# Kernel optimization log

Measured on AMD Instinct MI355X. Metric: run time of the kernel, lower is better.

## Reference

```python
import jax, jax.numpy as jnp
import numpy as np

B, FEAT, Q, L, H_ENC, H_DEC = 256, 64, 16, 2, 128, 256


def _apply_1q(state, U, q):
    # state: [B, 2,2,...,2] (Q qubit axes); U: [B,2,2] complex64
    s = jnp.moveaxis(state, 1 + q, 1)
    shp = s.shape
    s2 = s.reshape(shp[0], 2, -1)
    s2 = jnp.einsum('bij,bjr->bir', U, s2)
    return jnp.moveaxis(s2.reshape(shp), 1, 1 + q)


def _apply_cnot(state, c, t):
    # flip target axis on the control=1 slice
    c0 = jnp.take(state, 0, axis=1 + c)
    c1 = jnp.take(state, 1, axis=1 + c)
    t_ax = 1 + t if t < c else t  # target axis index after removing control axis
    c1 = jnp.flip(c1, axis=t_ax)
    return jnp.stack([c0, c1], axis=1 + c)


def _u3(theta, phi, lam):
    # combined Rz(lam) @ Ry(phi) @ Rx(theta); inputs [B] -> [B,2,2] complex64
    j = jnp.complex64(1j)
    ct, st = jnp.cos(theta / 2), jnp.sin(theta / 2)
    cp, sp = jnp.cos(phi / 2), jnp.sin(phi / 2)
    Rx = jnp.stack([jnp.stack([ct + 0j, -j * st], -1),
                    jnp.stack([-j * st, ct + 0j], -1)], -2)
    Ry = jnp.stack([jnp.stack([cp + 0j, -sp + 0j], -1),
                    jnp.stack([sp + 0j, cp + 0j], -1)], -2)
    em, ep = jnp.exp(-j * lam / 2), jnp.exp(j * lam / 2)
    zero = jnp.zeros_like(em)
    Rz = jnp.stack([jnp.stack([em, zero], -1),
                    jnp.stack([zero, ep], -1)], -2)
    return jnp.einsum('bij,bjk,bkl->bil', Rz, Ry, Rx).astype(jnp.complex64)


def setup_inputs() -> dict:
    key = jax.random.key(0)
    ks = jax.random.split(key, 6)

    def xavier(k, shape):
        lim = float(np.sqrt(6.0 / (shape[0] + shape[1])))
        return jax.random.uniform(k, shape, jnp.float32, -lim, lim)

    return {
        'x': jax.random.normal(ks[0], (B, FEAT), jnp.float32),
        'W1': xavier(ks[1], (FEAT, H_ENC)), 'b1': jnp.zeros((H_ENC,), jnp.float32),
        'W2': xavier(ks[2], (H_ENC, L * Q * 3)), 'b2': jnp.zeros((L * Q * 3,), jnp.float32),
        'scaling': jnp.ones((Q,), jnp.float32),
        'Wd1': xavier(ks[3], (2 ** Q, H_DEC)), 'bd1': jnp.zeros((H_DEC,), jnp.float32),
        'Wd2': xavier(ks[4], (H_DEC, FEAT)), 'bd2': jnp.zeros((FEAT,), jnp.float32),
    }


def reference(x, W1, b1, W2, b2, scaling, Wd1, bd1, Wd2, bd2):
    batch = x.shape[0]
    nq = scaling.shape[0]
    nl = W2.shape[1] // (nq * 3)
    # classical encoder -> quantum rotation angles
    h = jax.nn.relu(x @ W1 + b1)
    p = jnp.tanh(h @ W2 + b2).reshape(batch, nl, nq, 3)
    p = p * scaling[None, None, :, None] * jnp.pi  # theta/phi/lambda scaled by pi
    # batched statevector simulation, |0...0> init
    state = jnp.zeros((batch, 2 ** nq), jnp.complex64).at[:, 0].set(1.0)
    state = state.reshape((batch,) + (2,) * nq)
    for l in range(nl):
        for q in range(nq):
            U = _u3(p[:, l, q, 0], p[:, l, q, 1], p[:, l, q, 2])
            state = _apply_1q(state, U, q)
        if l < nl - 1:
            for q in range(nq - 1):
                state = _apply_cnot(state, q, q + 1)
            state = _apply_cnot(state, nq - 1, 0)
    probs = (jnp.real(state) ** 2 + jnp.imag(state) ** 2).reshape(batch, -1)
    # classical decoder
    out = jax.nn.relu(jax.nn.relu(probs @ Wd1 + bd1) @ Wd2 + bd2)
    return out
```

## Files before the change

kernel.cpp:

```cpp
#include <hip/hip_runtime.h>
#include <hip/hip_fp16.h>

#define PI_F 3.14159265358979323846f

typedef __attribute__((ext_vector_type(8))) _Float16 f16x8;
typedef __attribute__((ext_vector_type(16))) float f32x16;
typedef __attribute__((ext_vector_type(2))) float v2f;

__device__ __forceinline__ v2f pfma(v2f a, v2f b, v2f c) {
    return __builtin_elementwise_fma(a, b, c);
}
__device__ __forceinline__ v2f vswap(v2f a) { return __builtin_shufflevector(a, a, 1, 0); }
__device__ __forceinline__ v2f vsplat(float x) { v2f r; r.x = x; r.y = x; return r; }
__device__ __forceinline__ v2f mkc(v2f u) { v2f r; r.x = -u.y; r.y = u.y; return r; }
__device__ __forceinline__ v2f cmul(v2f a, v2f b) {
    return pfma(mkc(a), vswap(b), vsplat(a.x) * b);
}

__device__ __forceinline__ unsigned f2bf_rn(float x) {
    unsigned u = __float_as_uint(x);
    return (u + 0x7fffu + ((u >> 16) & 1u)) >> 16;
}

union H8 { int4 i4; f16x8 v; };

__device__ __forceinline__ void gll16(const void* g, void* l) {
    __builtin_amdgcn_global_load_lds(
        (const __attribute__((address_space(1))) void*)g,
        (__attribute__((address_space(3))) void*)l, 16, 0, 0);
}

union PreLds {
    struct {
        float xr[64]; float h[128]; float ang[96];
        v2f vL[32];
        v2f uL[64];
        _Float16 lR[256*8];
        _Float16 lL[512*8];
    } e;
    _Float16 wt[64][134];
};

__global__ __launch_bounds__(256) void k_pre(
        const float* __restrict__ x, const float* __restrict__ W1,
        const float* __restrict__ b1, const float* __restrict__ W2,
        const float* __restrict__ b2, const float* __restrict__ scaling,
        const float* __restrict__ Wd1, _Float16* __restrict__ Wt,
        _Float16* __restrict__ A) {
    __shared__ PreLds lds;
    const int t = threadIdx.x;
    if (blockIdx.x >= 256) {
        const int cb = blockIdx.x - 256;
        const int kb = (cb >> 2) * 128;
        const int nb = (cb & 3) * 64;
        unsigned* wtw = (unsigned*)&lds.wt[0][0];
        #pragma unroll
        for (int it = 0; it < 4; ++it) {
            int idx = t + it*256;
            int kr2 = idx >> 4;
            int nc4 = (idx & 15) * 4;
            const float* src = Wd1 + (size_t)(kb + 2*kr2)*256 + nb + nc4;
            float4 w0 = *(const float4*)src;
            float4 w1 = *(const float4*)(src + 256);
            #pragma unroll
            for (int j = 0; j < 4; ++j) {
                float a0 = (j==0?w0.x:j==1?w0.y:j==2?w0.z:w0.w) * 64.f;
                float a1 = (j==0?w1.x:j==1?w1.y:j==2?w1.z:w1.w) * 64.f;
                __half2 hh = __floats2half2_rn(a0, a1);
                unsigned u; __builtin_memcpy(&u, &hh, 4);
                wtw[(nc4 + j)*67 + kr2] = u;
            }
        }
        __syncthreads();
        #pragma unroll
        for (int it = 0; it < 4; ++it) {
            int idx = t + it*256;
            int n = idx >> 4, u = idx & 15;
            int4 hh = *(const int4*)&lds.wt[n][u*8];
            *(int4*)(Wt + ((size_t)(nb + n) << 16) + kb + u*8) = hh;
        }
        return;
    }
    const int b = blockIdx.x;
    if (t < 64) lds.e.xr[t] = x[b*64 + t];
    __syncthreads();
    if (t < 128) {
        float acc = b1[t];
        #pragma unroll 8
        for (int f = 0; f < 64; ++f) acc = fmaf(lds.e.xr[f], W1[f*128 + t], acc);
        lds.e.h[t] = fmaxf(acc, 0.f);
    }
    __syncthreads();
    if (t < 96) {
        float acc = b2[t];
        #pragma unroll 8
        for (int f = 0; f < 128; ++f) acc = fmaf(lds.e.h[f], W2[f*96 + t], acc);
        int q = (t/3) & 15;
        lds.e.ang[t] = tanhf(acc) * scaling[q] * PI_F;
    }
    __syncthreads();
    if (t < 32) {
        int l = t >> 4, q = t & 15;
        const float* a = lds.e.ang + l*48 + q*3;
        float st, ct, sp, cp, sl, cl;
        sincosf(a[0]*0.5f, &st, &ct);
        sincosf(a[1]*0.5f, &sp, &cp);
        sincosf(a[2]*0.5f, &sl, &cl);
        float2 A00 = make_float2( cp*ct,  sp*st);
        float2 A01 = make_float2(-sp*ct, -cp*st);
        float2 A10 = make_float2( sp*ct, -cp*st);
        float2 A11 = make_float2( cp*ct, -sp*st);
        float2 e0 = make_float2(cl, -sl), e1 = make_float2(cl, sl);
        v2f r00; r00.x = e0.x*A00.x - e0.y*A00.y; r00.y = e0.x*A00.y + e0.y*A00.x;
        v2f r01; r01.x = e0.x*A01.x - e0.y*A01.y; r01.y = e0.x*A01.y + e0.y*A01.x;
        v2f r10; r10.x = e1.x*A10.x - e1.y*A10.y; r10.y = e1.x*A10.y + e1.y*A10.x;
        v2f r11; r11.x = e1.x*A11.x - e1.y*A11.y; r11.y = e1.x*A11.y + e1.y*A11.x;
        if (l == 0) {
            lds.e.vL[q*2 + 0] = r00;
            lds.e.vL[q*2 + 1] = r10;
        } else {
            lds.e.uL[q*4 + 0] = r00; lds.e.uL[q*4 + 1] = r01;
            lds.e.uL[q*4 + 2] = r10; lds.e.uL[q*4 + 3] = r11;
        }
    }
    __syncthreads();
    #define AP(p, s) lds.e.vL[(15-(p))*2 + (s)]
    #define GG(p, zv, yv) lds.e.uL[(15-(p))*4 + (zv)*2 + (yv)]
    const float SL = 32.f;
    v2f Lg[2][2];
    {
        int z0 = t & 1, z1 = (t >> 1) & 1;
        #pragma unroll
        for (int g = 0; g < 2; ++g)
            #pragma unroll
            for (int y = 0; y < 2; ++y)
                Lg[g][y] = cmul(cmul(GG(0, z0, g), AP(0, g ^ y)), GG(1, z1, y));
        #pragma unroll
        for (int p = 2; p <= 7; ++p) {
            int zp = (t >> p) & 1;
            #pragma unroll
            for (int g = 0; g < 2; ++g) {
                v2f s0 = cmul(Lg[g][0], AP(p-1, 0)) + cmul(Lg[g][1], AP(p-1, 1));
                v2f s1 = cmul(Lg[g][0], AP(p-1, 1)) + cmul(Lg[g][1], AP(p-1, 0));
                Lg[g][0] = cmul(s0, GG(p, zp, 0));
                Lg[g][1] = cmul(s1, GG(p, zp, 1));
            }
        }
    }
    v2f Rg[2][2];
    {
        int z15 = (t >> 7) & 1;
        #pragma unroll
        for (int g = 0; g < 2; ++g)
            #pragma unroll
            for (int y14 = 0; y14 < 2; ++y14)
                Rg[g][y14] = cmul(cmul(AP(14, y14 ^ g),     AP(15, g)),     GG(15, z15, 0))
                           + cmul(cmul(AP(14, y14 ^ 1 ^ g), AP(15, 1 ^ g)), GG(15, z15, 1));
        #pragma unroll
        for (int p = 14; p >= 8; --p) {
            int zp = (t >> (p - 8)) & 1;
            #pragma unroll
            for (int g = 0; g < 2; ++g) {
                v2f t0 = cmul(GG(p, zp, 0), Rg[g][0]);
                v2f t1 = cmul(GG(p, zp, 1), Rg[g][1]);
                v2f n0 = cmul(AP(p-1, 0), t0) + cmul(AP(p-1, 1), t1);
                v2f n1 = cmul(AP(p-1, 1), t0) + cmul(AP(p-1, 0), t1);
                Rg[g][0] = n0; Rg[g][1] = n1;
            }
        }
    }
    #undef AP
    #undef GG
    {
        float lre[4] = {Lg[0][0].x, Lg[0][1].x, Lg[1][0].x, Lg[1][1].x};
        float lim[4] = {Lg[0][0].y, Lg[0][1].y, Lg[1][0].y, Lg[1][1].y};
        float rre[4] = {Rg[0][0].x, Rg[0][1].x, Rg[1][0].x, Rg[1][1].x};
        float rim[4] = {Rg[0][0].y, Rg[0][1].y, Rg[1][0].y, Rg[1][1].y};
        H8 hre, him, hr;
        #pragma unroll
        for (int k = 0; k < 4; ++k) {
            hre.v[k]   = (_Float16)(SL * lre[k]);
            hre.v[4+k] = (_Float16)(-SL * lim[k]);
            him.v[k]   = (_Float16)(SL * lim[k]);
            him.v[4+k] = (_Float16)(SL * lre[k]);
            hr.v[k]    = (_Float16)(SL * rre[k]);
            hr.v[4+k]  = (_Float16)(SL * rim[k]);
        }
        *(int4*)&lds.e.lR[t*8]         = hr.i4;
        *(int4*)&lds.e.lL[t*8]         = hre.i4;
        *(int4*)&lds.e.lL[(256+t)*8]   = him.i4;
    }
    __syncthreads();
    {
        const int wave = t >> 6, lane = t & 63, h2 = lane >> 5, l32 = lane & 31;
        f16x8 zf = {};
        _Float16* Aout = A + ((size_t)b << 16);
        #pragma unroll
        for (int mt2 = 0; mt2 < 2; ++mt2) {
            const int zh0 = (wave*2 + mt2)*32;
            f16x8 af = h2 ? zf : *(const f16x8*)&lds.e.lR[(zh0 + l32)*8];
            #pragma unroll
            for (int j = 0; j < 8; ++j) {
                f16x8 bre = h2 ? zf : *(const f16x8*)&lds.e.lL[(j*32 + l32)*8];
                f16x8 bim = h2 ? zf : *(const f16x8*)&lds.e.lL[(256 + j*32 + l32)*8];
                f32x16 zc = {};
                f32x16 dre = __builtin_amdgcn_mfma_f32_32x32x16_f16(af, bre, zc, 0, 0, 0);
                f32x16 dim = __builtin_amdgcn_mfma_f32_32x32x16_f16(af, bim, zc, 0, 0, 0);
                #pragma unroll
                for (int q = 0; q < 16; ++q) {
                    float p = fmaf(dre[q], dre[q], dim[q]*dim[q]) * 0.00390625f;
                    int row = zh0 + 4*h2 + (q & 3) + 8*(q >> 2);
                    Aout[row*256 + j*32 + l32] = (_Float16)p;
                }
            }
        }
    }
}

__global__ __launch_bounds__(256, 4) void k_gemm(
        const _Float16* __restrict__ A, const _Float16* __restrict__ Bt,
        unsigned short* __restrict__ partial) {
    __shared__ _Float16 lA[128*64];
    __shared__ _Float16 lB[128*64];
    const int id = blockIdx.x;
    const int ks = (id & 7) | ((id >> 5) << 3);
    const int p  = (id >> 3) & 3;
    const int nt = p >> 1, mt = p & 1;
    const int k0 = ks*256, n0 = nt*128, m0 = mt*128;
    const int tid = threadIdx.x, wave = tid >> 6, lane = tid & 63;
    const int mw = wave >> 1, nw = wave & 1;
    const int h = lane >> 5, l32 = lane & 31;
    f32x16 acc[2][2] = {};
    for (int s = 0; s < 4; ++s) {
        const int kb = k0 + s*64;
        #pragma unroll
        for (int i = 0; i < 4; ++i) {
            int ia = wave*4 + i;
            int r = ia*8 + (lane >> 3);
            int cch = (lane & 7) ^ (r & 7);
            gll16(A  + (size_t)(m0 + r)*65536 + kb + cch*8, &lA[ia*512]);
            gll16(Bt + (size_t)(n0 + r)*65536 + kb + cch*8, &lB[ia*512]);
        }
        __syncthreads();
        #pragma unroll
        for (int kk = 0; kk < 4; ++kk) {
            const int ch = kk*2 + h;
            f16x8 af[2], bf[2];
            #pragma unroll
            for (int xx = 0; xx < 2; ++xx) {
                int rA = mw*64 + xx*32 + l32;
                af[xx] = *(const f16x8*)&lA[rA*64 + ((ch ^ (rA & 7)) << 3)];
                int rB = nw*64 + xx*32 + l32;
                bf[xx] = *(const f16x8*)&lB[rB*64 + ((ch ^ (rB & 7)) << 3)];
            }
            #pragma unroll
            for (int i = 0; i < 2; ++i)
                #pragma unroll
                for (int jj = 0; jj < 2; ++jj)
                    acc[i][jj] = __builtin_amdgcn_mfma_f32_32x32x16_f16(af[i], bf[jj], acc[i][jj], 0, 0, 0);
        }
        __syncthreads();
    }
    unsigned short* pp = partial + (size_t)ks*65536;
    #pragma unroll
    for (int i = 0; i < 2; ++i) {
        #pragma unroll
        for (int jj = 0; jj < 2; ++jj) {
            int n = n0 + nw*64 + jj*32 + l32;
            int mb = m0 + mw*64 + i*32 + 4*h;
            #pragma unroll
            for (int q = 0; q < 16; ++q) {
                int m = mb + (q & 3) + 8*(q >> 2);
                pp[m*256 + n] = (unsigned short)f2bf_rn(acc[i][jj][q]);
            }
        }
    }
}

__global__ __launch_bounds__(256) void k_final(
        const unsigned short* __restrict__ partial, const float* __restrict__ bd1,
        const float* __restrict__ Wd2, const float* __restrict__ bd2,
        float* __restrict__ out) {
    __shared__ float row[256];
    const int m = blockIdx.x, t = threadIdx.x;
    {
        const unsigned short* p = partial + m*256 + t;
        float s = 0.f;
        #pragma unroll 32
        for (int kc = 0; kc < 256; ++kc)
            s += __uint_as_float(((unsigned)p[(size_t)kc*65536]) << 16);
        const float SC = 1.f / 262144.f;
        row[t] = fmaxf(fmaf(s, SC, bd1[t]), 0.f);
    }
    __syncthreads();
    if (t < 64) {
        float o = bd2[t];
        #pragma unroll 8
        for (int n = 0; n < 256; ++n) o = fmaf(row[n], Wd2[n*64 + t], o);
        out[m*64 + t] = fmaxf(o, 0.f);
    }
}

extern "C" void kernel_launch(void* const* d_in, const int* in_sizes, int n_in,
                              void* d_out, int out_size, void* d_ws, size_t ws_size,
                              hipStream_t stream) {
    const float* x       = (const float*)d_in[0];
    const float* W1      = (const float*)d_in[1];
    const float* b1      = (const float*)d_in[2];
    const float* W2      = (const float*)d_in[3];
    const float* b2      = (const float*)d_in[4];
    const float* scaling = (const float*)d_in[5];
    const float* Wd1     = (const float*)d_in[6];
    const float* bd1     = (const float*)d_in[7];
    const float* Wd2     = (const float*)d_in[8];
    const float* bd2     = (const float*)d_in[9];
    float* out = (float*)d_out;

    char* ws = (char*)d_ws;
    const size_t MB = 1024*1024;
    _Float16* A  = (_Float16*)(ws + 4*MB);
    _Float16* Wt = (_Float16*)(ws + 36*MB);
    unsigned short* partial = (unsigned short*)(ws + 68*MB);

    hipLaunchKernelGGL(k_pre, dim3(2304), dim3(256), 0, stream,
                       x, W1, b1, W2, b2, scaling, Wd1, Wt, A);
    hipLaunchKernelGGL(k_gemm, dim3(1024), dim3(256), 0, stream, A, Wt, partial);
    hipLaunchKernelGGL(k_final, dim3(256), dim3(256), 0, stream,
                       partial, bd1, Wd2, bd2, out);
}
```

Baseline: 170.6 us.

## Fuse Wd1 fp16 conversion into split-K GEMM and reorganize partial-sum layout

The separate k_pre blocks that transposed and converted Wd1 into an fp16 workspace are removed. k_gemm now loads Wd1 fp32 directly, converts and transposes it into swizzled LDS each k-step, and uses 512-thread blocks covering all 256 M rows with an n-half per block. The partial-sum layout is changed to m-major so that k_final reads contiguous 16-byte vectors and reduces them through LDS. This removes a 32MB workspace write and its re-read, at the cost of doing conversion work inside the GEMM loop and running half as many GEMM blocks.

```diff
diff --git a/kernel.cpp b/kernel.cpp
--- a/kernel.cpp
+++ b/kernel.cpp
@@ -23,6 +23,7 @@
 }
 
 union H8 { int4 i4; f16x8 v; };
+union U8 { int4 i4; unsigned short u[8]; };
 
 __device__ __forceinline__ void gll16(const void* g, void* l) {
     __builtin_amdgcn_global_load_lds(
@@ -30,78 +31,42 @@
         (__attribute__((address_space(3))) void*)l, 16, 0, 0);
 }
 
-union PreLds {
-    struct {
-        float xr[64]; float h[128]; float ang[96];
-        v2f vL[32];
-        v2f uL[64];
-        _Float16 lR[256*8];
-        _Float16 lL[512*8];
-    } e;
-    _Float16 wt[64][134];
+struct PreLds {
+    float xr[64]; float h[128]; float ang[96];
+    v2f vL[32];
+    v2f uL[64];
+    _Float16 lR[256*8];
+    _Float16 lL[512*8];
 };
 
 __global__ __launch_bounds__(256) void k_pre(
         const float* __restrict__ x, const float* __restrict__ W1,
         const float* __restrict__ b1, const float* __restrict__ W2,
         const float* __restrict__ b2, const float* __restrict__ scaling,
-        const float* __restrict__ Wd1, _Float16* __restrict__ Wt,
         _Float16* __restrict__ A) {
     __shared__ PreLds lds;
     const int t = threadIdx.x;
-    if (blockIdx.x >= 256) {
-        const int cb = blockIdx.x - 256;
-        const int kb = (cb >> 2) * 128;
-        const int nb = (cb & 3) * 64;
-        unsigned* wtw = (unsigned*)&lds.wt[0][0];
-        #pragma unroll
-        for (int it = 0; it < 4; ++it) {
-            int idx = t + it*256;
-            int kr2 = idx >> 4;
-            int nc4 = (idx & 15) * 4;
-            const float* src = Wd1 + (size_t)(kb + 2*kr2)*256 + nb + nc4;
-            float4 w0 = *(const float4*)src;
-            float4 w1 = *(const float4*)(src + 256);
-            #pragma unroll
-            for (int j = 0; j < 4; ++j) {
-                float a0 = (j==0?w0.x:j==1?w0.y:j==2?w0.z:w0.w) * 64.f;
-                float a1 = (j==0?w1.x:j==1?w1.y:j==2?w1.z:w1.w) * 64.f;
-                __half2 hh = __floats2half2_rn(a0, a1);
-                unsigned u; __builtin_memcpy(&u, &hh, 4);
-                wtw[(nc4 + j)*67 + kr2] = u;
-            }
-        }
-        __syncthreads();
-        #pragma unroll
-        for (int it = 0; it < 4; ++it) {
-            int idx = t + it*256;
-            int n = idx >> 4, u = idx & 15;
-            int4 hh = *(const int4*)&lds.wt[n][u*8];
-            *(int4*)(Wt + ((size_t)(nb + n) << 16) + kb + u*8) = hh;
-        }
-        return;
-    }
     const int b = blockIdx.x;
-    if (t < 64) lds.e.xr[t] = x[b*64 + t];
+    if (t < 64) lds.xr[t] = x[b*64 + t];
     __syncthreads();
     if (t < 128) {
         float acc = b1[t];
         #pragma unroll 8
-        for (int f = 0; f < 64; ++f) acc = fmaf(lds.e.xr[f], W1[f*128 + t], acc);
-        lds.e.h[t] = fmaxf(acc, 0.f);
+        for (int f = 0; f < 64; ++f) acc = fmaf(lds.xr[f], W1[f*128 + t], acc);
+        lds.h[t] = fmaxf(acc, 0.f);
     }
     __syncthreads();
     if (t < 96) {
         float acc = b2[t];
         #pragma unroll 8
-        for (int f = 0; f < 128; ++f) acc = fmaf(lds.e.h[f], W2[f*96 + t], acc);
+        for (int f = 0; f < 128; ++f) acc = fmaf(lds.h[f], W2[f*96 + t], acc);
         int q = (t/3) & 15;
-        lds.e.ang[t] = tanhf(acc) * scaling[q] * PI_F;
+        lds.ang[t] = tanhf(acc) * scaling[q] * PI_F;
     }
     __syncthreads();
     if (t < 32) {
         int l = t >> 4, q = t & 15;
-        const float* a = lds.e.ang + l*48 + q*3;
+        const float* a = lds.ang + l*48 + q*3;
         float st, ct, sp, cp, sl, cl;
         sincosf(a[0]*0.5f, &st, &ct);
         sincosf(a[1]*0.5f, &sp, &cp);
@@ -116,16 +81,16 @@
         v2f r10; r10.x = e1.x*A10.x - e1.y*A10.y; r10.y = e1.x*A10.y + e1.y*A10.x;
         v2f r11; r11.x = e1.x*A11.x - e1.y*A11.y; r11.y = e1.x*A11.y + e1.y*A11.x;
         if (l == 0) {
-            lds.e.vL[q*2 + 0] = r00;
-            lds.e.vL[q*2 + 1] = r10;
+            lds.vL[q*2 + 0] = r00;
+            lds.vL[q*2 + 1] = r10;
         } else {
-            lds.e.uL[q*4 + 0] = r00; lds.e.uL[q*4 + 1] = r01;
-            lds.e.uL[q*4 + 2] = r10; lds.e.uL[q*4 + 3] = r11;
-        }
-    }
-    __syncthreads();
-    #define AP(p, s) lds.e.vL[(15-(p))*2 + (s)]
-    #define GG(p, zv, yv) lds.e.uL[(15-(p))*4 + (zv)*2 + (yv)]
+            lds.uL[q*4 + 0] = r00; lds.uL[q*4 + 1] = r01;
+            lds.uL[q*4 + 2] = r10; lds.uL[q*4 + 3] = r11;
+        }
+    }
+    __syncthreads();
+    #define AP(p, s) lds.vL[(15-(p))*2 + (s)]
+    #define GG(p, zv, yv) lds.uL[(15-(p))*4 + (zv)*2 + (yv)]
     const float SL = 32.f;
     v2f Lg[2][2];
     {
@@ -186,9 +151,9 @@
             hr.v[k]    = (_Float16)(SL * rre[k]);
             hr.v[4+k]  = (_Float16)(SL * rim[k]);
         }
-        *(int4*)&lds.e.lR[t*8]         = hr.i4;
-        *(int4*)&lds.e.lL[t*8]         = hre.i4;
-        *(int4*)&lds.e.lL[(256+t)*8]   = him.i4;
+        *(int4*)&lds.lR[t*8]         = hr.i4;
+        *(int4*)&lds.lL[t*8]         = hre.i4;
+        *(int4*)&lds.lL[(256+t)*8]   = him.i4;
     }
     __syncthreads();
     {
@@ -198,11 +163,11 @@
         #pragma unroll
         for (int mt2 = 0; mt2 < 2; ++mt2) {
             const int zh0 = (wave*2 + mt2)*32;
-            f16x8 af = h2 ? zf : *(const f16x8*)&lds.e.lR[(zh0 + l32)*8];
+            f16x8 af = h2 ? zf : *(const f16x8*)&lds.lR[(zh0 + l32)*8];
             #pragma unroll
             for (int j = 0; j < 8; ++j) {
-                f16x8 bre = h2 ? zf : *(const f16x8*)&lds.e.lL[(j*32 + l32)*8];
-                f16x8 bim = h2 ? zf : *(const f16x8*)&lds.e.lL[(256 + j*32 + l32)*8];
+                f16x8 bre = h2 ? zf : *(const f16x8*)&lds.lL[(j*32 + l32)*8];
+                f16x8 bim = h2 ? zf : *(const f16x8*)&lds.lL[(256 + j*32 + l32)*8];
                 f32x16 zc = {};
                 f32x16 dre = __builtin_amdgcn_mfma_f32_32x32x16_f16(af, bre, zc, 0, 0, 0);
                 f32x16 dim = __builtin_amdgcn_mfma_f32_32x32x16_f16(af, bim, zc, 0, 0, 0);
@@ -217,29 +182,49 @@
     }
 }
 
-__global__ __launch_bounds__(256, 4) void k_gemm(
-        const _Float16* __restrict__ A, const _Float16* __restrict__ Bt,
+__global__ __launch_bounds__(512, 4) void k_gemm(
+        const _Float16* __restrict__ A, const float* __restrict__ Wd1,
         unsigned short* __restrict__ partial) {
-    __shared__ _Float16 lA[128*64];
+    __shared__ _Float16 lA[256*64];
     __shared__ _Float16 lB[128*64];
     const int id = blockIdx.x;
-    const int ks = (id & 7) | ((id >> 5) << 3);
-    const int p  = (id >> 3) & 3;
-    const int nt = p >> 1, mt = p & 1;
-    const int k0 = ks*256, n0 = nt*128, m0 = mt*128;
-    const int tid = threadIdx.x, wave = tid >> 6, lane = tid & 63;
+    const int xcd = id & 7, rr = id >> 3;
+    const int ks = xcd*32 + (rr & 31);
+    const int nh = rr >> 5;
+    const int k0 = ks*256, n0 = nh*128;
+    const int tid = threadIdx.x;
+    const int wave = tid >> 6, lane = tid & 63;
     const int mw = wave >> 1, nw = wave & 1;
     const int h = lane >> 5, l32 = lane & 31;
+    const int kw = tid >> 4;
+    const int nb8 = (tid & 15) * 8;
+    unsigned* lBw = (unsigned*)lB;
     f32x16 acc[2][2] = {};
     for (int s = 0; s < 4; ++s) {
         const int kb = k0 + s*64;
+        const float* wsrc = Wd1 + (size_t)(kb + 2*kw)*256 + n0 + nb8;
+        float4 w0a = *(const float4*)(wsrc);
+        float4 w0b = *(const float4*)(wsrc + 4);
+        float4 w1a = *(const float4*)(wsrc + 256);
+        float4 w1b = *(const float4*)(wsrc + 260);
         #pragma unroll
         for (int i = 0; i < 4; ++i) {
             int ia = wave*4 + i;
             int r = ia*8 + (lane >> 3);
             int cch = (lane & 7) ^ (r & 7);
-            gll16(A  + (size_t)(m0 + r)*65536 + kb + cch*8, &lA[ia*512]);
-            gll16(Bt + (size_t)(n0 + r)*65536 + kb + cch*8, &lB[ia*512]);
+            gll16(A + (size_t)r*65536 + kb + cch*8, &lA[ia*512]);
+        }
+        {
+            float a0[8] = {w0a.x,w0a.y,w0a.z,w0a.w,w0b.x,w0b.y,w0b.z,w0b.w};
+            float a1[8] = {w1a.x,w1a.y,w1a.z,w1a.w,w1b.x,w1b.y,w1b.z,w1b.w};
+            #pragma unroll
+            for (int j = 0; j < 8; ++j) {
+                int n = nb8 + j;
+                int S = ((n >> 3) & 7) ^ j;
+                __half2 hh = __floats2half2_rn(a0[j]*64.f, a1[j]*64.f);
+                unsigned u; __builtin_memcpy(&u, &hh, 4);
+                lBw[n*32 + (((kw >> 2) ^ S) << 2) + (kw & 3)] = u;
+            }
         }
         __syncthreads();
         #pragma unroll
@@ -251,7 +236,8 @@
                 int rA = mw*64 + xx*32 + l32;
                 af[xx] = *(const f16x8*)&lA[rA*64 + ((ch ^ (rA & 7)) << 3)];
                 int rB = nw*64 + xx*32 + l32;
-                bf[xx] = *(const f16x8*)&lB[rB*64 + ((ch ^ (rB & 7)) << 3)];
+                int SB = ((rB >> 3) & 7) ^ (rB & 7);
+                bf[xx] = *(const f16x8*)&lB[rB*64 + ((ch ^ SB) << 3)];
             }
             #pragma unroll
             for (int i = 0; i < 2; ++i)
@@ -261,17 +247,16 @@
         }
         __syncthreads();
     }
-    unsigned short* pp = partial + (size_t)ks*65536;
     #pragma unroll
     for (int i = 0; i < 2; ++i) {
         #pragma unroll
         for (int jj = 0; jj < 2; ++jj) {
             int n = n0 + nw*64 + jj*32 + l32;
-            int mb = m0 + mw*64 + i*32 + 4*h;
+            int mb = mw*64 + i*32 + 4*h;
             #pragma unroll
             for (int q = 0; q < 16; ++q) {
                 int m = mb + (q & 3) + 8*(q >> 2);
-                pp[m*256 + n] = (unsigned short)f2bf_rn(acc[i][jj][q]);
+                partial[((size_t)m*256 + ks)*256 + n] = (unsigned short)f2bf_rn(acc[i][jj][q]);
             }
         }
     }
@@ -281,23 +266,37 @@
         const unsigned short* __restrict__ partial, const float* __restrict__ bd1,
         const float* __restrict__ Wd2, const float* __restrict__ bd2,
         float* __restrict__ out) {
+    __shared__ float red[8][256];
     __shared__ float row[256];
     const int m = blockIdx.x, t = threadIdx.x;
-    {
-        const unsigned short* p = partial + m*256 + t;
+    const int o = t & 31, kg = t >> 5;
+    {
+        const unsigned short* p = partial + (size_t)m*65536 + kg*32*256 + o*8;
+        float acc[8] = {0.f,0.f,0.f,0.f,0.f,0.f,0.f,0.f};
+        #pragma unroll 8
+        for (int i = 0; i < 32; ++i) {
+            U8 v; v.i4 = *(const int4*)(p + (size_t)i*256);
+            #pragma unroll
+            for (int j = 0; j < 8; ++j)
+                acc[j] += __uint_as_float(((unsigned)v.u[j]) << 16);
+        }
+        #pragma unroll
+        for (int j = 0; j < 8; ++j) red[kg][o*8 + j] = acc[j];
+    }
+    __syncthreads();
+    {
         float s = 0.f;
-        #pragma unroll 32
-        for (int kc = 0; kc < 256; ++kc)
-            s += __uint_as_float(((unsigned)p[(size_t)kc*65536]) << 16);
+        #pragma unroll
+        for (int g = 0; g < 8; ++g) s += red[g][t];
         const float SC = 1.f / 262144.f;
         row[t] = fmaxf(fmaf(s, SC, bd1[t]), 0.f);
     }
     __syncthreads();
     if (t < 64) {
-        float o = bd2[t];
+        float o2 = bd2[t];
         #pragma unroll 8
-        for (int n = 0; n < 256; ++n) o = fmaf(row[n], Wd2[n*64 + t], o);
-        out[m*64 + t] = fmaxf(o, 0.f);
+        for (int n = 0; n < 256; ++n) o2 = fmaf(row[n], Wd2[n*64 + t], o2);
+        out[m*64 + t] = fmaxf(o2, 0.f);
     }
 }
 
@@ -319,12 +318,11 @@
     char* ws = (char*)d_ws;
     const size_t MB = 1024*1024;
     _Float16* A  = (_Float16*)(ws + 4*MB);
-    _Float16* Wt = (_Float16*)(ws + 36*MB);
-    unsigned short* partial = (unsigned short*)(ws + 68*MB);
-
-    hipLaunchKernelGGL(k_pre, dim3(2304), dim3(256), 0, stream,
-                       x, W1, b1, W2, b2, scaling, Wd1, Wt, A);
-    hipLaunchKernelGGL(k_gemm, dim3(1024), dim3(256), 0, stream, A, Wt, partial);
+    unsigned short* partial = (unsigned short*)(ws + 36*MB);
+
+    hipLaunchKernelGGL(k_pre, dim3(256), dim3(256), 0, stream,
+                       x, W1, b1, W2, b2, scaling, A);
+    hipLaunchKernelGGL(k_gemm, dim3(512), dim3(512), 0, stream, A, Wd1, partial);
     hipLaunchKernelGGL(k_final, dim3(256), dim3(256), 0, stream,
                        partial, bd1, Wd2, bd2, out);
 }
```

Measured after the change: 169.0 us. About the same (-1.0%).
